# Performance work log

Measured on AMD Instinct MI355X. Metric: run time of the kernel, lower is better.

## Reference

```python
import jax, jax.numpy as jnp
import numpy as np

B, L, K = 256, 2048, 8
INV_SQRT2 = 0.7071067811865476


def _scalar_mul(d1, d2):
    # (a + b*w + c*w^2 + d*w^3)*(a' + ...) in Z[omega], omega = e^{i pi/4}, w^4 = -1
    a1, b1, c1, e1 = d1[..., 0], d1[..., 1], d1[..., 2], d1[..., 3]
    a2, b2, c2, e2 = d2[..., 0], d2[..., 1], d2[..., 2], d2[..., 3]
    A = a1 * a2 + b1 * e2 - c1 * c2 + e1 * b2
    Bc = a1 * b2 + b1 * a2 + c1 * e2 + e1 * c2
    C = a1 * c2 + b1 * b2 + c1 * a2 - e1 * e2
    D = a1 * e2 - b1 * c2 - c1 * b2 + e1 * a2
    return jnp.stack([A, Bc, C, D], axis=-1).astype(d1.dtype)


def setup_inputs() -> dict:
    key = jax.random.key(0)
    k1, k2, k3, k4 = jax.random.split(key, 4)
    coeffs1 = jax.random.randint(k1, (B, L, K, 4), 0, 2).astype(jnp.float32)
    coeffs2 = jax.random.randint(k2, (B, L, K, 4), 0, 2).astype(jnp.float32)
    power1 = jax.random.randint(k3, (B, L, K), 0, 2, dtype=jnp.int32)
    power2 = jax.random.randint(k4, (B, L, K), 0, 2, dtype=jnp.int32)
    return {"coeffs1": coeffs1, "coeffs2": coeffs2, "power1": power1, "power2": power2}


def reference(coeffs1, coeffs2, power1, power2):
    # __mul__: elementwise ring multiply, powers add
    z = _scalar_mul(coeffs1, coeffs2)          # [B,L,K,4]
    zp = power1 + power2                        # [B,L,K]

    # reduce(): divide coeffs by 2 while all even (and nonzero), bump power
    def cond_fun(carry):
        c, _ = carry
        red = jnp.all(c % 2 == 0, axis=-1) & jnp.any(c != 0, axis=-1)
        return jnp.any(red)

    def body_fun(carry):
        c, p = carry
        red = jnp.all(c % 2 == 0, axis=-1) & jnp.any(c != 0, axis=-1)
        c = jnp.where(red[..., None], c // 2, c)
        p = jnp.where(red, p + 1, p)
        return (c, p)

    c, p = jax.lax.while_loop(cond_fun, body_fun, (z, zp))

    # prod(axis=2): associative scan of the ring multiply, take last; powers sum
    scanned = jax.lax.associative_scan(_scalar_mul, c, axis=2)
    pc = scanned[:, :, -1, :]                   # [B,L,4]
    pp = jnp.sum(p, axis=2)                     # [B,L]

    # sum(): align powers to the min over L (axis=-2 of coeffs), then sum
    minp = jnp.min(pp, axis=-1)                 # [B]
    align = (2.0 ** (pp - minp[..., None])).astype(pc.dtype)
    sc = jnp.sum(pc * align[..., None], axis=-2)  # [B,4]

    # to_complex(): c0 + c1*e^{i pi/4} + c2*i + c3*e^{-i pi/4}, scaled by 2^power
    real = sc[..., 0] + (sc[..., 1] + sc[..., 3]) * INV_SQRT2
    imag = sc[..., 2] + (sc[..., 1] - sc[..., 3]) * INV_SQRT2
    scale = (2.0 ** minp).astype(sc.dtype)
    return jnp.stack([real * scale, imag * scale], axis=-1)  # [B,2] (real, imag)
```

## Files before the change

### kernel.cpp

```cpp
#include <hip/hip_runtime.h>

constexpr int BB = 256;
constexpr int LL = 2048;
constexpr int KK = 8;
constexpr int THREADS = 512;
constexpr int SPLIT = 4;
constexpr double INV_SQRT2 = 0.7071067811865476;


__device__ __forceinline__ void ring_mul(int& ra, int& rb, int& rc, int& rd,
                                         int A, int Bv, int C, int D) {
    const int nA = __mul24(ra, A)  + __mul24(rb, D)  - __mul24(rc, C)  + __mul24(rd, Bv);
    const int nB = __mul24(ra, Bv) + __mul24(rb, A)  + __mul24(rc, D)  + __mul24(rd, C);
    const int nC = __mul24(ra, C)  + __mul24(rb, Bv) + __mul24(rc, A)  - __mul24(rd, D);
    const int nD = __mul24(ra, D)  - __mul24(rb, C)  - __mul24(rc, Bv) + __mul24(rd, A);
    ra = nA; rb = nB; rc = nC; rd = nD;
}

__device__ __forceinline__ void process(const float4 u, const float4 v, int p,
                                        const int lane, double& accR, double& accI) {
    const int a1 = (int)u.x, b1 = (int)u.y, g1 = (int)u.z, e1 = (int)u.w;
    const int a2 = (int)v.x, b2 = (int)v.y, g2 = (int)v.z, e2 = (int)v.w;

    int A  = __mul24(a1,a2) + __mul24(b1,e2) - __mul24(g1,g2) + __mul24(e1,b2);
    int Bv = __mul24(a1,b2) + __mul24(b1,a2) + __mul24(g1,e2) + __mul24(e1,g2);
    int C  = __mul24(a1,g2) + __mul24(b1,b2) + __mul24(g1,a2) - __mul24(e1,e2);
    int D  = __mul24(a1,e2) - __mul24(b1,g2) - __mul24(g1,b2) + __mul24(e1,a2);

    const int m = A | Bv | C | D;
    const int s = (m == 0) ? 0 : __builtin_ctz(m);
    A >>= s; Bv >>= s; C >>= s; D >>= s;
    p += s;

    #pragma unroll
    for (int off = 1; off < 8; off <<= 1) {
        const int oa = __shfl_xor(A,  off, 64);
        const int ob = __shfl_xor(Bv, off, 64);
        const int oc = __shfl_xor(C,  off, 64);
        const int od = __shfl_xor(D,  off, 64);
        const int op = __shfl_xor(p,  off, 64);
        ring_mul(A, Bv, C, D, oa, ob, oc, od);
        p += op;
    }

    const unsigned long long bits = ((unsigned long long)(1023 + p)) << 52;
    const double w = ((lane & 7) == 0) ? __longlong_as_double((long long)bits) : 0.0;
    const double dA = (double)A, dB = (double)Bv, dC = (double)C, dD = (double)D;
    accR += w * (dA + (dB + dD) * INV_SQRT2);
    accI += w * (dC + (dB - dD) * INV_SQRT2);
}

__global__ __launch_bounds__(THREADS, 8) void esa_kernel(
    const float4* __restrict__ c1,
    const float4* __restrict__ c2,
    const int*  __restrict__ p1,
    const int*  __restrict__ p2,
    float* __restrict__ out) {
    const int b    = blockIdx.x >> 2;
    const int part = blockIdx.x & 3;
    const int tid  = threadIdx.x;
    const int wave = tid >> 6;
    const int lane = tid & 63;

    constexpr int LSPAN = LL / SPLIT;
    constexpr int GRP   = 4;
    constexpr int LPW   = 8 * GRP;
    constexpr int LPB   = (THREADS / 64) * LPW;
    constexpr int ITERS = LSPAN / LPB;

    double accR = 0.0, accI = 0.0;

    for (int it = 0; it < ITERS; ++it) {
        const int lbase = part * LSPAN + it * LPB + wave * LPW;
        const long long i0 = ((long long)b * LL + lbase) * KK + lane;

        float4 u[GRP], v[GRP]; int pw[GRP];
        #pragma unroll
        for (int g = 0; g < GRP; ++g) {
            const long long idx = i0 + (long long)g * 64;
            u[g]  = c1[idx];
            v[g]  = c2[idx];
            pw[g] = p1[idx] + p2[idx];
        }

        #pragma unroll
        for (int g = 0; g < GRP; ++g)
            process(u[g], v[g], pw[g], lane, accR, accI);
    }

    for (int off = 32; off > 0; off >>= 1) {
        accR += __shfl_down(accR, off, 64);
        accI += __shfl_down(accI, off, 64);
    }
    __shared__ double sR[THREADS / 64], sI[THREADS / 64];
    if (lane == 0) { sR[wave] = accR; sI[wave] = accI; }
    __syncthreads();
    if (tid == 0) {
        double tR = 0.0, tI = 0.0;
        #pragma unroll
        for (int w = 0; w < THREADS / 64; ++w) { tR += sR[w]; tI += sI[w]; }
        atomicAdd(&out[b * 2 + 0], (float)tR);
        atomicAdd(&out[b * 2 + 1], (float)tI);
    }
}

extern "C" void kernel_launch(void* const* d_in, const int* in_sizes, int n_in,
                              void* d_out, int out_size, void* d_ws, size_t ws_size,
                              hipStream_t stream) {
    const float4* c1 = (const float4*)d_in[0];
    const float4* c2 = (const float4*)d_in[1];
    const int*    p1 = (const int*)d_in[2];
    const int*    p2 = (const int*)d_in[3];
    float* out = (float*)d_out;

    hipMemsetAsync(out, 0, (size_t)out_size * sizeof(float), stream);
    esa_kernel<<<BB * SPLIT, THREADS, 0, stream>>>(c1, c2, p1, p2, out);
}
```

Before: 36.41 us.

## Software-pipeline loads with register double buffering and smaller group size

Restructures the main loop so the next tile's coefficient and power loads are issued before the current tile is processed. This double-buffers in registers to overlap global memory latency with the ring-multiply and shuffle work. The group size drops from 4 to 2, which doubles ITERS and fully unrolls the loop. The launch-bounds occupancy hint is lowered from 8 to 6 to leave room for the extra live registers, at the risk of fewer resident waves hiding latency.

```diff
diff --git a/kernel.cpp b/kernel.cpp
--- a/kernel.cpp
+++ b/kernel.cpp
@@ -50,7 +50,25 @@
     accI += w * (dC + (dB - dD) * INV_SQRT2);
 }
 
-__global__ __launch_bounds__(THREADS, 8) void esa_kernel(
+struct Tile {
+    float4 u0, v0, u1, v1;
+    int pa0, pb0, pa1, pb1;
+};
+
+__device__ __forceinline__ Tile load_tile(const float4* __restrict__ c1,
+                                          const float4* __restrict__ c2,
+                                          const int* __restrict__ p1,
+                                          const int* __restrict__ p2,
+                                          long long i0) {
+    Tile t;
+    t.u0 = c1[i0];       t.v0 = c2[i0];
+    t.u1 = c1[i0 + 64];  t.v1 = c2[i0 + 64];
+    t.pa0 = p1[i0];      t.pb0 = p2[i0];
+    t.pa1 = p1[i0 + 64]; t.pb1 = p2[i0 + 64];
+    return t;
+}
+
+__global__ __launch_bounds__(THREADS, 6) void esa_kernel(
     const float4* __restrict__ c1,
     const float4* __restrict__ c2,
     const int*  __restrict__ p1,
@@ -63,29 +81,24 @@
     const int lane = tid & 63;
 
     constexpr int LSPAN = LL / SPLIT;
-    constexpr int GRP   = 4;
+    constexpr int GRP   = 2;
     constexpr int LPW   = 8 * GRP;
     constexpr int LPB   = (THREADS / 64) * LPW;
     constexpr int ITERS = LSPAN / LPB;
 
     double accR = 0.0, accI = 0.0;
 
+    const long long i0 = ((long long)b * LL + part * LSPAN + wave * LPW) * KK + lane;
+
+    Tile cur = load_tile(c1, c2, p1, p2, i0);
+    #pragma unroll
     for (int it = 0; it < ITERS; ++it) {
-        const int lbase = part * LSPAN + it * LPB + wave * LPW;
-        const long long i0 = ((long long)b * LL + lbase) * KK + lane;
-
-        float4 u[GRP], v[GRP]; int pw[GRP];
-        #pragma unroll
-        for (int g = 0; g < GRP; ++g) {
-            const long long idx = i0 + (long long)g * 64;
-            u[g]  = c1[idx];
-            v[g]  = c2[idx];
-            pw[g] = p1[idx] + p2[idx];
-        }
-
-        #pragma unroll
-        for (int g = 0; g < GRP; ++g)
-            process(u[g], v[g], pw[g], lane, accR, accI);
+        Tile nxt;
+        if (it + 1 < ITERS)
+            nxt = load_tile(c1, c2, p1, p2, i0 + (long long)(it + 1) * LPB * KK);
+        process(cur.u0, cur.v0, cur.pa0 + cur.pb0, lane, accR, accI);
+        process(cur.u1, cur.v1, cur.pa1 + cur.pb1, lane, accR, accI);
+        if (it + 1 < ITERS) cur = nxt;
     }
 
     for (int off = 32; off > 0; off >>= 1) {
```

Result: no change. 36.46 us (+0.2%).
